# Optimization experiments

Measured on AMD Instinct MI355X. Metric: run time of the kernel, lower is better.

## Reference

```python
import jax, jax.numpy as jnp
import numpy as np

B, I, O = 1024, 512, 512
EPS = 1e-07
LOG_CLIP = 20.0

def setup_inputs() -> dict:
    key = jax.random.key(0)
    k1, k2, k3, k4 = jax.random.split(key, 4)
    x = jax.random.normal(k1, (B, I), dtype=jnp.float32)
    # match tf.random_normal_initializer(mean, stddev) used in the layer
    w_hat = 0.88 + 0.2 * jax.random.normal(k2, (I, O), dtype=jnp.float32)
    m_hat = 0.5 + 0.2 * jax.random.normal(k3, (I, O), dtype=jnp.float32)
    g = 0.2 * jax.random.normal(k4, (O,), dtype=jnp.float32)
    return {"x": x, "w_hat": w_hat, "m_hat": m_hat, "g": g}

def reference(x, w_hat, m_hat, g):
    w1 = jnp.tanh(w_hat) * jax.nn.sigmoid(m_hat)          # [I, O]
    a = x @ w1                                             # [B, O] additive path
    # multiplicative path: exp(log|x| @ w1), clipped at 20 before exp
    logx = jnp.log(jnp.maximum(jnp.abs(x), EPS))           # [B, I]
    m1 = jnp.exp(jnp.minimum(logx @ w1, LOG_CLIP))         # [B, O]
    # sign-product tracking. TF flattens w1 row-major to [I*O], tiles x
    # O times along axis 1 -> xs[b, k] = x[b, k % I]; so after reshape to
    # [B, O, I], the paired weight magnitude is ws[j, i] = |w1.flat[j*I + i]|.
    ws_oi = jnp.abs(w1.reshape(-1)).reshape(O, I)          # [O, I] (faithful to TF reshape)
    sgn_x = jnp.sign(x)                                    # [B, I]
    sgn = sgn_x[:, None, :] * ws_oi[None, :, :] + (1.0 - ws_oi)[None, :, :]  # [B, O, I]
    ms = jnp.prod(sgn, axis=2)                             # [B, O]
    g1 = jax.nn.sigmoid(g)                                 # [O]
    return g1 * a + (1.0 - g1) * m1 * jnp.clip(ms, -1.0, 1.0)
```

## Files before the change

kernel.cpp:

```cpp
#include <hip/hip_runtime.h>


#define O_N 512
#define I_N 512
#define B_N 1024

typedef _Float16 f16;
typedef _Float16 f16x8 __attribute__((ext_vector_type(8)));
typedef float f32x4 __attribute__((ext_vector_type(4)));

__device__ __forceinline__ float fast_sigmoid(float v) {
    return 1.0f / (1.0f + __expf(-v));
}
__device__ __forceinline__ float fast_tanh(float v) {
    return 1.0f - 2.0f / (1.0f + __expf(2.0f * v));
}

__global__ __launch_bounds__(256) void prep_kernel(const float* __restrict__ x,
                                                   const float* __restrict__ wh,
                                                   const float* __restrict__ mh,
                                                   f16x8* __restrict__ apx,
                                                   f16x8* __restrict__ apl,
                                                   f16x8* __restrict__ bp) {
    const int tid = threadIdx.x;
    if (blockIdx.x < 128) {
        __shared__ f16 lt[32][72];
        const int kb = blockIdx.x >> 3;
        const int nb = blockIdx.x & 7;
        const int r  = tid >> 3;
        const int c0 = (tid & 7) * 8;
        const int base = (kb * 32 + r) * O_N + nb * 64 + c0;
        const float4* w4 = (const float4*)(wh + base);
        const float4* m4 = (const float4*)(mh + base);
        const float4 wa = w4[0], wb = w4[1], ma = m4[0], mb = m4[1];
        f16x8 row;
        row[0] = (f16)(fast_tanh(wa.x) * fast_sigmoid(ma.x));
        row[1] = (f16)(fast_tanh(wa.y) * fast_sigmoid(ma.y));
        row[2] = (f16)(fast_tanh(wa.z) * fast_sigmoid(ma.z));
        row[3] = (f16)(fast_tanh(wa.w) * fast_sigmoid(ma.w));
        row[4] = (f16)(fast_tanh(wb.x) * fast_sigmoid(mb.x));
        row[5] = (f16)(fast_tanh(wb.y) * fast_sigmoid(mb.y));
        row[6] = (f16)(fast_tanh(wb.z) * fast_sigmoid(mb.z));
        row[7] = (f16)(fast_tanh(wb.w) * fast_sigmoid(mb.w));
        *(f16x8*)&lt[r][c0] = row;
        __syncthreads();
        const int fl  = tid & 63;
        const int tnl = tid >> 6;
        const int nl  = tnl * 16 + (fl & 15);
        const int k0  = (fl >> 4) * 8;
        f16x8 bf;
#pragma unroll
        for (int j = 0; j < 8; ++j) bf[j] = lt[k0 + j][nl];
        const int tn_g = nb * 4 + tnl;
        bp[tn_g * 1024 + kb * 64 + fl] = bf;
    } else {
        const int t  = (blockIdx.x - 128) * 256 + tid;
        const int fl = t & 63;
        const int tk = (t >> 6) & 15;
        const int tm = t >> 10;
        const int m  = tm * 16 + (fl & 15);
        const int k0 = tk * 32 + (fl >> 4) * 8;
        const float4* x4 = (const float4*)(x + m * I_N + k0);
        const float4 q0 = x4[0], q1 = x4[1];
        const float vx[8] = {q0.x, q0.y, q0.z, q0.w, q1.x, q1.y, q1.z, q1.w};
        f16x8 fx, fv;
#pragma unroll
        for (int j = 0; j < 8; ++j) {
            fx[j] = (f16)vx[j];
            fv[j] = (f16)__logf(fmaxf(fabsf(vx[j]), 1e-7f));
        }
        apx[t] = fx;
        apl[t] = fv;
    }
}

__global__ __launch_bounds__(256) void nalu_mfma_kernel(const f16x8* __restrict__ apx,
                                                        const f16x8* __restrict__ apl,
                                                        const f16x8* __restrict__ bp,
                                                        const float* __restrict__ g,
                                                        const float* __restrict__ x,
                                                        const float* __restrict__ wh,
                                                        const float* __restrict__ mh,
                                                        float* __restrict__ out) {
    const int lane = threadIdx.x & 63;
    const int w    = threadIdx.x >> 6;
    const int b0   = blockIdx.y * 32 + (w & 1) * 16;
    const int o0   = blockIdx.x * 32 + (w >> 1) * 16;
    const int tm   = b0 >> 4;
    const int tn   = o0 >> 4;

    f32x4 ca = {0.f, 0.f, 0.f, 0.f}, cs = ca;

    const f16x8* pax = apx + tm * 1024 + lane;
    const f16x8* pal = apl + tm * 1024 + lane;
    const f16x8* pbp = bp  + tn * 1024 + lane;

#pragma unroll 8
    for (int tk = 0; tk < 16; ++tk) {
        const f16x8 ax = pax[tk * 64];
        const f16x8 al = pal[tk * 64];
        const f16x8 bf = pbp[tk * 64];
        ca = __builtin_amdgcn_mfma_f32_16x16x32_f16(ax, bf, ca, 0, 0, 0);
        cs = __builtin_amdgcn_mfma_f32_16x16x32_f16(al, bf, cs, 0, 0, 0);
    }

    const int col = lane & 15;
    const int rq  = (lane >> 4) * 4;
    const int o   = o0 + col;
    const float g1  = fast_sigmoid(g[o]);
    const float omg = 1.0f - g1;
#pragma unroll
    for (int r = 0; r < 4; ++r) {
        const int b = b0 + rq + r;
        const float sv = cs[r];
        const float m1 = __expf(fminf(sv, 20.0f));
        float msv = 1.0f;
        if (sv > -80.0f) {
            float p = 1.0f;
            for (int i = 0; i < I_N; ++i) {
                const float wv = fabsf(fast_tanh(wh[o * I_N + i]) *
                                       fast_sigmoid(mh[o * I_N + i]));
                const float xv = x[b * I_N + i];
                const float sg = (xv > 0.f) ? 1.f : ((xv < 0.f) ? -1.f : 0.f);
                p *= sg * wv + (1.0f - wv);
            }
            msv = fminf(fmaxf(p, -1.0f), 1.0f);
        }
        out[b * O_N + o] = g1 * ca[r] + omg * m1 * msv;
    }
}

extern "C" void kernel_launch(void* const* d_in, const int* in_sizes, int n_in,
                              void* d_out, int out_size, void* d_ws, size_t ws_size,
                              hipStream_t stream) {
    const float* x  = (const float*)d_in[0];
    const float* wh = (const float*)d_in[1];
    const float* mh = (const float*)d_in[2];
    const float* g  = (const float*)d_in[3];
    float* out = (float*)d_out;

    char* ws = (char*)d_ws;
    f16x8* apx = (f16x8*)ws;
    f16x8* apl = (f16x8*)(ws + (1u << 20));
    f16x8* bp  = (f16x8*)(ws + (2u << 20));

    prep_kernel<<<384, 256, 0, stream>>>(x, wh, mh, apx, apl, bp);
    nalu_mfma_kernel<<<dim3(16, 32), 256, 0, stream>>>(apx, apl, bp, g, x, wh, mh, out);
}
```

Before: 68.22 us.

## Coalesce x prep loads via LDS staging and swizzle main-kernel block order

```diff
diff --git a/kernel.cpp b/kernel.cpp
--- a/kernel.cpp
+++ b/kernel.cpp
@@ -22,9 +22,10 @@
                                                    f16x8* __restrict__ apx,
                                                    f16x8* __restrict__ apl,
                                                    f16x8* __restrict__ bp) {
+    __shared__ __align__(16) f16 sh[2 * 16 * 520];
     const int tid = threadIdx.x;
     if (blockIdx.x < 128) {
-        __shared__ f16 lt[32][72];
+        f16 (*lt)[72] = (f16 (*)[72])sh;
         const int kb = blockIdx.x >> 3;
         const int nb = blockIdx.x & 7;
         const int r  = tid >> 3;
@@ -54,23 +55,37 @@
         const int tn_g = nb * 4 + tnl;
         bp[tn_g * 1024 + kb * 64 + fl] = bf;
     } else {
-        const int t  = (blockIdx.x - 128) * 256 + tid;
-        const int fl = t & 63;
-        const int tk = (t >> 6) & 15;
-        const int tm = t >> 10;
-        const int m  = tm * 16 + (fl & 15);
-        const int k0 = tk * 32 + (fl >> 4) * 8;
-        const float4* x4 = (const float4*)(x + m * I_N + k0);
-        const float4 q0 = x4[0], q1 = x4[1];
-        const float vx[8] = {q0.x, q0.y, q0.z, q0.w, q1.x, q1.y, q1.z, q1.w};
-        f16x8 fx, fv;
+        const int blk = blockIdx.x - 128;
+        f16* lxA = sh;
+        f16* lxB = sh + 16 * 520;
 #pragma unroll
-        for (int j = 0; j < 8; ++j) {
-            fx[j] = (f16)vx[j];
-            fv[j] = (f16)__logf(fmaxf(fabsf(vx[j]), 1e-7f));
+        for (int p = 0; p < 4; ++p) {
+            const int e = p * 2048 + tid * 8;
+            const float4* x4 = (const float4*)(x + blk * 8192 + e);
+            const float4 q0 = x4[0], q1 = x4[1];
+            const float vx[8] = {q0.x, q0.y, q0.z, q0.w, q1.x, q1.y, q1.z, q1.w};
+            const int ml = e >> 9;
+            const int k  = e & 511;
+            f16x8 fx, fv;
+#pragma unroll
+            for (int j = 0; j < 8; ++j) {
+                fx[j] = (f16)vx[j];
+                fv[j] = (f16)__logf(fmaxf(fabsf(vx[j]), 1e-7f));
+            }
+            *(f16x8*)&lxA[ml * 520 + k] = fx;
+            *(f16x8*)&lxB[ml * 520 + k] = fv;
         }
-        apx[t] = fx;
-        apl[t] = fv;
+        __syncthreads();
+#pragma unroll
+        for (int p = 0; p < 4; ++p) {
+            const int s  = p * 256 + tid;
+            const int tk = s >> 6;
+            const int fl = s & 63;
+            const int ml = fl & 15;
+            const int k0 = tk * 32 + (fl >> 4) * 8;
+            apx[blk * 1024 + s] = *(const f16x8*)&lxA[ml * 520 + k0];
+            apl[blk * 1024 + s] = *(const f16x8*)&lxB[ml * 520 + k0];
+        }
     }
 }
 
@@ -82,10 +97,15 @@
                                                         const float* __restrict__ wh,
                                                         const float* __restrict__ mh,
                                                         float* __restrict__ out) {
+    const int bid = blockIdx.x;
+    const int swz = (bid & 7) * 64 + (bid >> 3);
+    const int oT  = swz & 15;
+    const int bT  = swz >> 4;
+
     const int lane = threadIdx.x & 63;
     const int w    = threadIdx.x >> 6;
-    const int b0   = blockIdx.y * 32 + (w & 1) * 16;
-    const int o0   = blockIdx.x * 32 + (w >> 1) * 16;
+    const int b0   = bT * 32 + (w & 1) * 16;
+    const int o0   = oT * 32 + (w >> 1) * 16;
     const int tm   = b0 >> 4;
     const int tn   = o0 >> 4;
 
@@ -144,6 +164,6 @@
     f16x8* apl = (f16x8*)(ws + (1u << 20));
     f16x8* bp  = (f16x8*)(ws + (2u << 20));
 
-    prep_kernel<<<384, 256, 0, stream>>>(x, wh, mh, apx, apl, bp);
-    nalu_mfma_kernel<<<dim3(16, 32), 256, 0, stream>>>(apx, apl, bp, g, x, wh, mh, out);
+    prep_kernel<<<192, 256, 0, stream>>>(x, wh, mh, apx, apl, bp);
+    nalu_mfma_kernel<<<512, 256, 0, stream>>>(apx, apl, bp, g, x, wh, mh, out);
 }
```

Measured after the change: 68.14 us. About the same (-0.1%).
